# Optimization experiments

Measured on AMD Instinct MI355X. Metric: run time of the kernel, lower is better.

Reference implementation:

```python
import jax, jax.numpy as jnp
import numpy as np

N, E, B = 40000, 640000, 8192
IN, META, HID, OUT = 768, 6, 256, 128
NE, K, REL, NET = 4, 2, 200, 3
NL, NH, FF = 4, 4, 512


def setup_inputs():
    key = jax.random.key(0)
    keys = iter(jax.random.split(key, 64))
    def p(*shape):
        return jax.random.normal(next(keys), shape, jnp.float32) * 0.02
    return dict(
        x=jax.random.normal(next(keys), (N, IN + META), jnp.float32),
        noise=jax.random.normal(next(keys), (3, B, NE), jnp.float32),
        g_lin1_w=p(HID, IN + META), g_lin1_b=p(HID),
        conv_W=p(2, HID, HID), conv_Wr=p(2, HID, REL), conv_a=p(2, 3 * HID),
        conv_Wres=p(2, HID, HID), conv_rel=p(2, NET, REL),
        g_lin2_w=p(OUT, HID), g_lin2_b=p(OUT),
        te_w=p(OUT, IN), te_b=p(OUT),
        me_w1=p(HID, META), me_b1=p(HID), me_w2=p(OUT, HID), me_b2=p(OUT),
        moe_gate_w=p(3, NE, OUT), moe_noise_w=p(3, OUT),
        moe_w1=p(3, NE, 4 * OUT, OUT), moe_b1=p(3, NE, 4 * OUT),
        moe_w2=p(3, NE, OUT, 4 * OUT), moe_b2=p(3, NE, OUT),
        tf_qkv_w=p(NL, 3 * OUT, OUT), tf_qkv_b=p(NL, 3 * OUT),
        tf_out_w=p(NL, OUT, OUT), tf_out_b=p(NL, OUT),
        tf_ln1_g=jnp.ones((NL, OUT), jnp.float32), tf_ln1_b=jnp.zeros((NL, OUT), jnp.float32),
        tf_ff1_w=p(NL, FF, OUT), tf_ff1_b=p(NL, FF),
        tf_ff2_w=p(NL, OUT, FF), tf_ff2_b=p(NL, OUT),
        tf_ln2_g=jnp.ones((NL, OUT), jnp.float32), tf_ln2_b=jnp.zeros((NL, OUT), jnp.float32),
        clf_w=p(2, 3 * OUT), clf_b=p(2),
        edge_index=jax.random.randint(next(keys), (2, E), 0, N),
        edge_type=jax.random.randint(next(keys), (E,), 0, NET),
        batch_size=B,
    )


def _seg_softmax(logit, seg, n):
    m = jax.ops.segment_max(logit, seg, num_segments=n)
    e = jnp.exp(logit - m[seg])
    s = jax.ops.segment_sum(e, seg, num_segments=n)
    return e / (s[seg] + 1e-16)


def _hgn_layer(h, src, dst, et, W, Wr, a, Wres, rel, final):
    n, d = h.shape[0], W.shape[0]
    Wx = h @ W.T  # [N, HID]
    # a(cat(Wx_i, Wx_j, Wr_rel)) decomposed: per-node + per-edge-type scalars
    s_i = Wx @ a[:d]
    s_j = Wx @ a[d:2 * d]
    r_s = (rel @ Wr.T) @ a[2 * d:]  # [NET]
    logit = jax.nn.leaky_relu(s_i[dst] + s_j[src] + r_s[et], 0.2)
    alpha = _seg_softmax(logit, dst, n)
    agg = jax.ops.segment_sum(Wx[src] * alpha[:, None], dst, num_segments=n)
    out = jax.nn.elu(agg + h @ Wres.T)
    if final:
        out = out / jnp.maximum(jnp.linalg.norm(out, axis=1, keepdims=True), 1e-12)
    return out


def _moe(xv, eps, gate_w, noise_w, w1, b1, w2, b2):
    g = xv @ gate_w.T                       # [B, NE]
    nsd = jax.nn.softplus(xv @ noise_w)     # [B]
    h = g + eps * nsd[:, None]
    _, bot = jax.lax.top_k(-h, K)           # bottom-K experts get -inf
    drop = jnp.sum(jax.nn.one_hot(bot, NE, dtype=h.dtype), axis=1) > 0
    h = jnp.where(drop, -jnp.inf, h)
    L = jax.nn.softmax(h, axis=1)
    logits, idx = jax.lax.top_k(L, K)
    tmp = L.sum(0)
    loss = (jnp.std(tmp, ddof=1) / jnp.mean(tmp)) ** 2
    comb = jnp.einsum('bs,bse->be', logits, jax.nn.one_hot(idx, NE, dtype=L.dtype))
    h1 = jax.nn.relu(jnp.einsum('bd,ehd->ebh', xv, w1) + b1[:, None, :])
    eo = jnp.einsum('ebh,eoh->ebo', h1, w2) + b2[:, None, :]  # [NE, B, OUT]
    return jnp.einsum('be,ebo->bo', comb, eo), loss


def _ln(x, g, b):
    mu = x.mean(-1, keepdims=True)
    var = x.var(-1, keepdims=True)
    return (x - mu) / jnp.sqrt(var + 1e-5) * g + b


def _tf_layer(x, qkv_w, qkv_b, out_w, out_b, ln1g, ln1b, f1w, f1b, f2w, f2b, ln2g, ln2b):
    Bq, S, D = x.shape
    hd = D // NH
    qkv = x @ qkv_w.T + qkv_b
    q, k, v = jnp.split(qkv, 3, axis=-1)
    q = q.reshape(Bq, S, NH, hd)
    k = k.reshape(Bq, S, NH, hd)
    v = v.reshape(Bq, S, NH, hd)
    att = jax.nn.softmax(jnp.einsum('bshd,bthd->bhst', q, k) / jnp.sqrt(jnp.float32(hd)), axis=-1)
    o = jnp.einsum('bhst,bthd->bshd', att, v).reshape(Bq, S, D)
    x = _ln(x + o @ out_w.T + out_b, ln1g, ln1b)
    ff = jax.nn.relu(x @ f1w.T + f1b) @ f2w.T + f2b
    return _ln(x + ff, ln2g, ln2b)


def _forward(x, noise, g_lin1_w, g_lin1_b, conv_W, conv_Wr, conv_a, conv_Wres, conv_rel,
             g_lin2_w, g_lin2_b, te_w, te_b, me_w1, me_b1, me_w2, me_b2,
             moe_gate_w, moe_noise_w, moe_w1, moe_b1, moe_w2, moe_b2,
             tf_qkv_w, tf_qkv_b, tf_out_w, tf_out_b, tf_ln1_g, tf_ln1_b,
             tf_ff1_w, tf_ff1_b, tf_ff2_w, tf_ff2_b, tf_ln2_g, tf_ln2_b,
             clf_w, clf_b, edge_index, edge_type, batch_size):
    src, dst = edge_index[0], edge_index[1]
    # graph encoder (dropout is eval no-op)
    h = jax.nn.relu(x @ g_lin1_w.T + g_lin1_b)
    h = _hgn_layer(h, src, dst, edge_type, conv_W[0], conv_Wr[0], conv_a[0], conv_Wres[0], conv_rel[0], False)
    h = _hgn_layer(h, src, dst, edge_type, conv_W[1], conv_Wr[1], conv_a[1], conv_Wres[1], conv_rel[1], True)
    graph = jax.nn.relu(h @ g_lin2_w.T + g_lin2_b)
    x_g = graph[:batch_size]
    text = x[:batch_size, :IN]
    meta = x[:batch_size, IN:]
    x_t = jax.nn.relu(text @ te_w.T + te_b)
    x_m = jax.nn.relu(jax.nn.relu(meta @ me_w1.T + me_b1) @ me_w2.T + me_b2)
    outs, losses = [], []
    for i, xv in enumerate((x_g, x_t, x_m)):
        o, l = _moe(xv, noise[i], moe_gate_w[i], moe_noise_w[i], moe_w1[i], moe_b1[i], moe_w2[i], moe_b2[i])
        outs.append(o)
        losses.append(l)
    loss = losses[0] + losses[1] + losses[2]
    z = jnp.stack(outs, axis=1)  # [B, 3, OUT]
    for li in range(NL):
        z = _tf_layer(z, tf_qkv_w[li], tf_qkv_b[li], tf_out_w[li], tf_out_b[li],
                      tf_ln1_g[li], tf_ln1_b[li], tf_ff1_w[li], tf_ff1_b[li],
                      tf_ff2_w[li], tf_ff2_b[li], tf_ln2_g[li], tf_ln2_b[li])
    logits = z.reshape(z.shape[0], -1) @ clf_w.T + clf_b
    return logits, loss


def reference(x, noise, g_lin1_w, g_lin1_b, conv_W, conv_Wr, conv_a, conv_Wres, conv_rel,
              g_lin2_w, g_lin2_b, te_w, te_b, me_w1, me_b1, me_w2, me_b2,
              moe_gate_w, moe_noise_w, moe_w1, moe_b1, moe_w2, moe_b2,
              tf_qkv_w, tf_qkv_b, tf_out_w, tf_out_b, tf_ln1_g, tf_ln1_b,
              tf_ff1_w, tf_ff1_b, tf_ff2_w, tf_ff2_b, tf_ln2_g, tf_ln2_b,
              clf_w, clf_b, edge_index, edge_type, batch_size):
    return _forward(x, noise, g_lin1_w, g_lin1_b, conv_W, conv_Wr, conv_a, conv_Wres, conv_rel,
                    g_lin2_w, g_lin2_b, te_w, te_b, me_w1, me_b1, me_w2, me_b2,
                    moe_gate_w, moe_noise_w, moe_w1, moe_b1, moe_w2, moe_b2,
                    tf_qkv_w, tf_qkv_b, tf_out_w, tf_out_b, tf_ln1_g, tf_ln1_b,
                    tf_ff1_w, tf_ff1_b, tf_ff2_w, tf_ff2_b, tf_ln2_g, tf_ln2_b,
                    clf_w, clf_b, edge_index, edge_type, batch_size)
```

## Files before the change

### kernel.cpp

```cpp
#include <hip/hip_runtime.h>
#include <hip/hip_bf16.h>
#include <math.h>

#define NN 40000
#define EE 640000
#define BB 8192
#define IN_DIM 768
#define META_DIM 6
#define XDIM 774
#define HID 256
#define OUT_D 128
#define NEXP 4
#define NET_T 3
#define REL_D 200
#define NLAY 4
#define FF_D 512

typedef __attribute__((ext_vector_type(8))) short short8;
typedef __attribute__((ext_vector_type(4))) float f32x4;

__device__ __forceinline__ ushort f2bf(float f) {
    union { float f; unsigned u; } a; a.f = f;
    unsigned u = a.u;
    unsigned r = (u + 0x7FFFu + ((u >> 16) & 1u)) >> 16;
    return (ushort)r;
}
__device__ __forceinline__ float bf2f(ushort h) {
    union { unsigned u; float f; } a; a.u = ((unsigned)h) << 16;
    return a.f;
}

__global__ void cvt_kernel(const float* __restrict__ src, int ldsrc, int Kreal,
                           ushort* __restrict__ hi, ushort* __restrict__ lo,
                           int R, int ldp)
{
    size_t i = (size_t)blockIdx.x * blockDim.x + threadIdx.x;
    size_t total = (size_t)R * ldp;
    if (i >= total) return;
    int col = (int)(i % ldp);
    int row = (int)(i / ldp);
    float v = (col < Kreal) ? src[(size_t)row * ldsrc + col] : 0.f;
    ushort h = f2bf(v);
    float rem = v - bf2f(h);
    hi[i] = h;
    lo[i] = f2bf(rem);
}

static void cvt(const float* src, int ldsrc, int Kreal, ushort* hi, ushort* lo,
                int R, int ldp, hipStream_t s)
{
    size_t total = (size_t)R * ldp;
    cvt_kernel<<<(int)((total + 255) / 256), 256, 0, s>>>(src, ldsrc, Kreal, hi, lo, R, ldp);
}

template<int ACT, int HAS_RES>
__global__ __launch_bounds__(256) void mfma_gemm3(
    const ushort* __restrict__ Ahi, const ushort* __restrict__ Alo, int lda,
    const ushort* __restrict__ Bhi, const ushort* __restrict__ Blo, int ldb,
    const float* __restrict__ bias, const float* __restrict__ res,
    float* __restrict__ C, int M, int Nn, int K)
{
    __shared__ __align__(16) ushort Ash[128 * 40];
    __shared__ __align__(16) ushort Asl[128 * 40];
    __shared__ __align__(16) ushort Bsh[64 * 40];
    __shared__ __align__(16) ushort Bsl[64 * 40];

    int bn = blockIdx.x * 64;
    int bm = blockIdx.y * 128;
    int t = threadIdx.x;
    int wave = t >> 6, lane = t & 63;
    int wm = wave & 1, wn = wave >> 1;
    int quad = lane >> 4, r = lane & 15;

    f32x4 acc[4][2];
#pragma unroll
    for (int i = 0; i < 4; i++)
#pragma unroll
        for (int j = 0; j < 2; j++) acc[i][j] = (f32x4){0.f, 0.f, 0.f, 0.f};

    for (int k0 = 0; k0 < K; k0 += 32) {
#pragma unroll
        for (int i = 0; i < 2; i++) {
            int idx = t + i * 256;
            int row = idx >> 2, c8 = idx & 3;
            int grow = bm + row; if (grow > M - 1) grow = M - 1;
            size_t off = (size_t)grow * lda + k0 + c8 * 8;
            *(short8*)&Ash[row * 40 + c8 * 8] = *(const short8*)(Ahi + off);
            *(short8*)&Asl[row * 40 + c8 * 8] = *(const short8*)(Alo + off);
        }
        {
            int row = t >> 2, c8 = t & 3;
            size_t off = (size_t)(bn + row) * ldb + k0 + c8 * 8;
            *(short8*)&Bsh[row * 40 + c8 * 8] = *(const short8*)(Bhi + off);
            *(short8*)&Bsl[row * 40 + c8 * 8] = *(const short8*)(Blo + off);
        }
        __syncthreads();

        short8 ah[4], al[4], bh[2], bl[2];
#pragma unroll
        for (int i = 0; i < 4; i++) {
            int ro = (wm * 64 + i * 16 + r) * 40 + quad * 8;
            ah[i] = *(const short8*)&Ash[ro];
            al[i] = *(const short8*)&Asl[ro];
        }
#pragma unroll
        for (int j = 0; j < 2; j++) {
            int ro = (wn * 32 + j * 16 + r) * 40 + quad * 8;
            bh[j] = *(const short8*)&Bsh[ro];
            bl[j] = *(const short8*)&Bsl[ro];
        }
#pragma unroll
        for (int i = 0; i < 4; i++)
#pragma unroll
            for (int j = 0; j < 2; j++)
                acc[i][j] = __builtin_amdgcn_mfma_f32_16x16x32_bf16(ah[i], bh[j], acc[i][j], 0, 0, 0);
#pragma unroll
        for (int i = 0; i < 4; i++)
#pragma unroll
            for (int j = 0; j < 2; j++)
                acc[i][j] = __builtin_amdgcn_mfma_f32_16x16x32_bf16(ah[i], bl[j], acc[i][j], 0, 0, 0);
#pragma unroll
        for (int i = 0; i < 4; i++)
#pragma unroll
            for (int j = 0; j < 2; j++)
                acc[i][j] = __builtin_amdgcn_mfma_f32_16x16x32_bf16(al[i], bh[j], acc[i][j], 0, 0, 0);
        __syncthreads();
    }

    float bcol[2];
#pragma unroll
    for (int j = 0; j < 2; j++)
        bcol[j] = bias ? bias[bn + wn * 32 + j * 16 + r] : 0.f;
#pragma unroll
    for (int i = 0; i < 4; i++) {
#pragma unroll
        for (int j = 0; j < 2; j++) {
            int col = bn + wn * 32 + j * 16 + r;
#pragma unroll
            for (int reg = 0; reg < 4; reg++) {
                int row = bm + wm * 64 + i * 16 + quad * 4 + reg;
                if (row >= M) continue;
                float v = acc[i][j][reg] + bcol[j];
                if (HAS_RES) v += res[(size_t)row * Nn + col];
                if (ACT == 1) v = fmaxf(v, 0.f);
                else if (ACT == 2) v = (v > 0.f) ? v : expm1f(v);
                C[(size_t)row * Nn + col] = v;
            }
        }
    }
}

template<int ACT, int HAS_RES>
static void mfma3_launch(const ushort* Ahi, const ushort* Alo, int lda,
                         const ushort* Bhi, const ushort* Blo, int ldb,
                         const float* bias, const float* res, float* C,
                         int M, int Nn, int K, hipStream_t s)
{
    dim3 grid(Nn / 64, (M + 127) / 128);
    mfma_gemm3<ACT, HAS_RES><<<grid, 256, 0, s>>>(Ahi, Alo, lda, Bhi, Blo, ldb,
                                                  bias, res, C, M, Nn, K);
}

template<int ACT>
__global__ void gemm_kernel(const float* __restrict__ A, int lda,
                            const float* __restrict__ Bw,
                            const float* __restrict__ bias,
                            const float* __restrict__ res,
                            float* __restrict__ C, int M, int Nn, int K)
{
    __shared__ float As[16][68];
    __shared__ float Bs[16][68];
    int bm = blockIdx.y * 64, bn = blockIdx.x * 64;
    int t = threadIdx.x;
    int tx = t & 15, ty = t >> 4;
    float acc[4][4] = {{0.f}};

    for (int k0 = 0; k0 < K; k0 += 16) {
#pragma unroll
        for (int i = 0; i < 4; i++) {
            int l = t * 4 + i; int mm = l >> 4, kk = l & 15;
            int gm = bm + mm, gk = k0 + kk;
            As[kk][mm] = (gm < M && gk < K) ? A[(size_t)gm * lda + gk] : 0.f;
        }
#pragma unroll
        for (int i = 0; i < 4; i++) {
            int l = t * 4 + i; int nn = l >> 4, kk = l & 15;
            int gn = bn + nn, gk = k0 + kk;
            Bs[kk][nn] = (gn < Nn && gk < K) ? Bw[(size_t)gn * K + gk] : 0.f;
        }
        __syncthreads();
#pragma unroll
        for (int kk = 0; kk < 16; kk++) {
            float4 a4 = *reinterpret_cast<const float4*>(&As[kk][ty * 4]);
            float4 b4 = *reinterpret_cast<const float4*>(&Bs[kk][tx * 4]);
            float a0[4] = {a4.x, a4.y, a4.z, a4.w};
            float b0[4] = {b4.x, b4.y, b4.z, b4.w};
#pragma unroll
            for (int i = 0; i < 4; i++)
#pragma unroll
                for (int j = 0; j < 4; j++)
                    acc[i][j] += a0[i] * b0[j];
        }
        __syncthreads();
    }
#pragma unroll
    for (int i = 0; i < 4; i++) {
        int gm = bm + ty * 4 + i; if (gm >= M) continue;
#pragma unroll
        for (int j = 0; j < 4; j++) {
            int gn = bn + tx * 4 + j; if (gn >= Nn) continue;
            float v = acc[i][j];
            if (bias) v += bias[gn];
            if (res)  v += res[(size_t)gm * Nn + gn];
            if (ACT == 1) v = fmaxf(v, 0.f);
            else if (ACT == 2) v = (v > 0.f) ? v : expm1f(v);
            C[(size_t)gm * Nn + gn] = v;
        }
    }
}

static void launch_gemm(int act, const float* A, int lda, const float* Bw,
                        const float* bias, const float* res, float* C,
                        int M, int Nn, int K, hipStream_t s)
{
    dim3 grid((Nn + 63) / 64, (M + 63) / 64);
    dim3 blk(256);
    if (act == 0)      gemm_kernel<0><<<grid, blk, 0, s>>>(A, lda, Bw, bias, res, C, M, Nn, K);
    else if (act == 1) gemm_kernel<1><<<grid, blk, 0, s>>>(A, lda, Bw, bias, res, C, M, Nn, K);
    else               gemm_kernel<2><<<grid, blk, 0, s>>>(A, lda, Bw, bias, res, C, M, Nn, K);
}

template<int ACT, int A_BF16, int OUT_BF16>
__global__ __launch_bounds__(256) void mfma_gemm(
    const void* __restrict__ Ap, size_t strideAz,
    const float* __restrict__ Bw, size_t strideBz,
    const float* __restrict__ bias, size_t strideBiasz,
    void* __restrict__ Cp, size_t strideCz,
    int M, int Nn, int K)
{
    __shared__ __align__(16) ushort As[128 * 40];
    __shared__ __align__(16) ushort Bs[64 * 40];

    int z = blockIdx.z;
// ... 142 lines not shown
        buf[t] = v;
        __syncthreads();
        for (int off = 1; off < 1024; off <<= 1) {
            int x = (t >= off) ? buf[t - off] : 0;
            __syncthreads();
            buf[t] += x;
            __syncthreads();
        }
        int incl = buf[t];
        int base = carry;
        if (c + t < n) { rowstart[c + t] = base + incl - v; cursor[c + t] = base + incl - v; }
        __syncthreads();
        if (t == 1023) carry = base + incl;
        __syncthreads();
    }
    if (t == 0) rowstart[n] = carry;
}

__global__ void fill_kernel(const int* __restrict__ src, const int* __restrict__ dst,
                            const int* __restrict__ et, int* __restrict__ cursor,
                            unsigned* __restrict__ csr_val)
{
    int e = blockIdx.x * blockDim.x + threadIdx.x;
    if (e >= EE) return;
    int d = dst[e];
    int pos = atomicAdd(&cursor[d], 1);
    csr_val[pos] = (unsigned)src[e] | ((unsigned)et[e] << 16);
}

__global__ void csr_agg_kernel(const unsigned* __restrict__ csr_val,
                               const int* __restrict__ rowstart,
                               const float* __restrict__ s_i, const float* __restrict__ s_j,
                               const float* __restrict__ rsv,
                               const float* __restrict__ Wx, float* __restrict__ agg)
{
    int t = threadIdx.x; int w = t >> 6, l = t & 63;
    int node = blockIdx.x * 4 + w; if (node >= NN) return;
    int start = rowstart[node], end = rowstart[node + 1];
    float r0 = rsv[0], r1 = rsv[1], r2 = rsv[2];
    float si = s_i[node];

    float m = -INFINITY;
    for (int i = start + l; i < end; i += 64) {
        unsigned v = csr_val[i];
        int s = v & 0xFFFF; int et = v >> 16;
        float rr = (et == 0) ? r0 : ((et == 1) ? r1 : r2);
        float lg = si + s_j[s] + rr;
        lg = (lg >= 0.f) ? lg : 0.2f * lg;
        m = fmaxf(m, lg);
    }
    for (int off = 32; off; off >>= 1) m = fmaxf(m, __shfl_down(m, off));
    m = __shfl(m, 0);

    float a0 = 0.f, a1 = 0.f, a2 = 0.f, a3 = 0.f, ssum = 0.f;
    for (int c = start; c < end; c += 64) {
        int nchunk = min(64, end - c);
        float wgt = 0.f; int sidx = 0;
        if (l < nchunk) {
            unsigned v = csr_val[c + l];
            sidx = v & 0xFFFF; int et = v >> 16;
            float rr = (et == 0) ? r0 : ((et == 1) ? r1 : r2);
            float lg = si + s_j[sidx] + rr;
            lg = (lg >= 0.f) ? lg : 0.2f * lg;
            wgt = expf(lg - m);
            ssum += wgt;
        }
        for (int j = 0; j < nchunk; j++) {
            float wj = __shfl(wgt, j);
            int sj = __shfl(sidx, j);
            const float* wr = Wx + (size_t)sj * HID;
            a0 += wj * wr[l];
            a1 += wj * wr[l + 64];
            a2 += wj * wr[l + 128];
            a3 += wj * wr[l + 192];
        }
    }
    for (int off = 32; off; off >>= 1) ssum += __shfl_down(ssum, off);
    ssum = __shfl(ssum, 0);
    float inv = 1.f / (ssum + 1e-16f);
    float* ar = agg + (size_t)node * HID;
    ar[l] = a0 * inv; ar[l + 64] = a1 * inv; ar[l + 128] = a2 * inv; ar[l + 192] = a3 * inv;
}

__global__ void rownorm_kernel(float* __restrict__ h, int n)
{
    int t = threadIdx.x; int w = t >> 6, l = t & 63;
    int m = blockIdx.x * 4 + w; if (m >= n) return;
    float* r = h + (size_t)m * HID;
    float vals[4]; float q = 0.f;
#pragma unroll
    for (int i = 0; i < 4; i++) { vals[i] = r[l + 64 * i]; q += vals[i] * vals[i]; }
    for (int off = 32; off; off >>= 1) q += __shfl_down(q, off);
    q = __shfl(q, 0);
    float inv = 1.f / fmaxf(sqrtf(q), 1e-12f);
#pragma unroll
    for (int i = 0; i < 4; i++) r[l + 64 * i] = vals[i] * inv;
}

__global__ void moe_gate_kernel(const float* __restrict__ xv, const float* __restrict__ gate_w,
                                const float* __restrict__ noise_w, const float* __restrict__ eps,
                                float* __restrict__ comb, float* __restrict__ tmpsum)
{
    __shared__ float part[4];
    int t = threadIdx.x; int w = t >> 6, l = t & 63;
    if (t < 4) part[t] = 0.f;
    __syncthreads();
    int b = blockIdx.x * 4 + w;
    const float* xr = xv + (size_t)b * OUT_D;
    float x0 = xr[l], x1 = xr[l + 64];
    float dots[5];
#pragma unroll
    for (int e = 0; e < 4; e++) {
        const float* gw = gate_w + e * OUT_D;
        float v = x0 * gw[l] + x1 * gw[l + 64];
        for (int off = 32; off; off >>= 1) v += __shfl_down(v, off);
        dots[e] = v;
    }
    {
        float v = x0 * noise_w[l] + x1 * noise_w[l + 64];
        for (int off = 32; off; off >>= 1) v += __shfl_down(v, off);
        dots[4] = v;
    }
    if (l == 0) {
        float xg = dots[4];
        float nsd = (xg > 20.f) ? xg : log1pf(expf(xg));
        float hv[4];
#pragma unroll
        for (int e = 0; e < 4; e++) hv[e] = dots[e] + eps[(size_t)b * 4 + e] * nsd;
        int i1 = 0;
        for (int e = 1; e < 4; e++) if (hv[e] < hv[i1]) i1 = e;
        int i2 = -1;
        for (int e = 0; e < 4; e++) { if (e == i1) continue; if (i2 < 0 || hv[e] < hv[i2]) i2 = e; }
        int k1 = -1, k2 = -1;
        for (int e = 0; e < 4; e++) { if (e != i1 && e != i2) { if (k1 < 0) k1 = e; else k2 = e; } }
        float mm = fmaxf(hv[k1], hv[k2]);
        float e1 = expf(hv[k1] - mm), e2 = expf(hv[k2] - mm);
        float s = e1 + e2;
        float L[4] = {0.f, 0.f, 0.f, 0.f};
        L[k1] = e1 / s; L[k2] = e2 / s;
#pragma unroll
        for (int e = 0; e < 4; e++) comb[(size_t)b * 4 + e] = L[e];
        atomicAdd(&part[k1], L[k1]);
        atomicAdd(&part[k2], L[k2]);
    }
    __syncthreads();
    if (t < 4) atomicAdd(&tmpsum[t], part[t]);
}

__global__ void moe_combine_kernel(const float* __restrict__ eo, const float* __restrict__ comb,
                                   float* __restrict__ zout)
{
    int idx = blockIdx.x * blockDim.x + threadIdx.x;
    if (idx >= BB * OUT_D) return;
    int b = idx >> 7, o = idx & 127;
    const size_t S = (size_t)BB * OUT_D;
    float v = comb[b * 4 + 0] * eo[idx] + comb[b * 4 + 1] * eo[idx + S]
            + comb[b * 4 + 2] * eo[idx + 2 * S] + comb[b * 4 + 3] * eo[idx + 3 * S];
    zout[(size_t)b * (3 * OUT_D) + o] = v;
}

__global__ void loss_kernel(const float* __restrict__ tmpsum, float* __restrict__ out)
{
    if (threadIdx.x == 0 && blockIdx.x == 0) {
        float total = 0.f;
        for (int v = 0; v < 3; v++) {
            const float* tp = tmpsum + v * 4;
            float mean = (tp[0] + tp[1] + tp[2] + tp[3]) * 0.25f;
            float var = 0.f;
            for (int e = 0; e < 4; e++) { float d = tp[e] - mean; var += d * d; }
            var /= 3.f;
            float r = sqrtf(var) / mean;
            total += r * r;
        }
        out[0] = total;
    }
}

__global__ void attn_kernel(const float* __restrict__ qkv, float* __restrict__ o)
{
// ... 42 lines not shown
    float v0 = xr[l] + ar[l], v1 = xr[l + 64] + ar[l + 64];
    float s = v0 + v1;
    for (int off = 32; off; off >>= 1) s += __shfl_down(s, off);
    s = __shfl(s, 0);
    float mu = s * (1.f / 128.f);
    float d0 = v0 - mu, d1 = v1 - mu;
    float q = d0 * d0 + d1 * d1;
    for (int off = 32; off; off >>= 1) q += __shfl_down(q, off);
    q = __shfl(q, 0);
    float inv = rsqrtf(q * (1.f / 128.f) + 1e-5f);
    xr[l]      = d0 * inv * g[l] + bta[l];
    xr[l + 64] = d1 * inv * g[l + 64] + bta[l + 64];
}

__global__ void clf_kernel(const float* __restrict__ z, const float* __restrict__ w,
                           const float* __restrict__ b, float* __restrict__ out)
{
    int t = threadIdx.x; int wv = t >> 6, l = t & 63;
    int row = blockIdx.x * 4 + wv; if (row >= BB) return;
    const float* zr = z + (size_t)row * 384;
    float v0 = 0.f, v1 = 0.f;
    for (int i = l; i < 384; i += 64) {
        float zz = zr[i];
        v0 += zz * w[i];
        v1 += zz * w[384 + i];
    }
    for (int off = 32; off; off >>= 1) { v0 += __shfl_down(v0, off); v1 += __shfl_down(v1, off); }
    if (l == 0) { out[row * 2] = v0 + b[0]; out[row * 2 + 1] = v1 + b[1]; }
}

extern "C" void kernel_launch(void* const* d_in, const int* in_sizes, int n_in,
                              void* d_out, int out_size, void* d_ws, size_t ws_size,
                              hipStream_t stream)
{
    const float* x         = (const float*)d_in[0];
    const float* noise     = (const float*)d_in[1];
    const float* g_lin1_w  = (const float*)d_in[2];
    const float* g_lin1_b  = (const float*)d_in[3];
    const float* conv_W    = (const float*)d_in[4];
    const float* conv_Wr   = (const float*)d_in[5];
    const float* conv_a    = (const float*)d_in[6];
    const float* conv_Wres = (const float*)d_in[7];
    const float* conv_rel  = (const float*)d_in[8];
    const float* g_lin2_w  = (const float*)d_in[9];
    const float* g_lin2_b  = (const float*)d_in[10];
    const float* te_w      = (const float*)d_in[11];
    const float* te_b      = (const float*)d_in[12];
    const float* me_w1     = (const float*)d_in[13];
    const float* me_b1     = (const float*)d_in[14];
    const float* me_w2     = (const float*)d_in[15];
    const float* me_b2     = (const float*)d_in[16];
    const float* moe_gate_w  = (const float*)d_in[17];
    const float* moe_noise_w = (const float*)d_in[18];
    const float* moe_w1    = (const float*)d_in[19];
    const float* moe_b1    = (const float*)d_in[20];
    const float* moe_w2    = (const float*)d_in[21];
    const float* moe_b2    = (const float*)d_in[22];
    const float* tf_qkv_w  = (const float*)d_in[23];
    const float* tf_qkv_b  = (const float*)d_in[24];
    const float* tf_out_w  = (const float*)d_in[25];
    const float* tf_out_b  = (const float*)d_in[26];
    const float* tf_ln1_g  = (const float*)d_in[27];
    const float* tf_ln1_b  = (const float*)d_in[28];
    const float* tf_ff1_w  = (const float*)d_in[29];
    const float* tf_ff1_b  = (const float*)d_in[30];
    const float* tf_ff2_w  = (const float*)d_in[31];
    const float* tf_ff2_b  = (const float*)d_in[32];
    const float* tf_ln2_g  = (const float*)d_in[33];
    const float* tf_ln2_b  = (const float*)d_in[34];
    const float* clf_w     = (const float*)d_in[35];
    const float* clf_b     = (const float*)d_in[36];
    const int*   edge_index = (const int*)d_in[37];
    const int*   edge_type  = (const int*)d_in[38];

    float* ws = (float*)d_ws;

    const size_t F_A = 0;
    const size_t F_B = 10240000;
    const size_t F_C = 22822912;
    const size_t F_D = 33062912;
    const size_t F_M = 43302912;
    const size_t F_X = 44200000;

    float* h0     = ws + F_A;
    float* qkv    = ws + F_A;
    float* wx     = ws + F_B;
    float* graph  = ws + F_B;
    ushort* ff1bf = (ushort*)(ws + F_B);
    float* agg    = ws + F_C;
    float* x_mh   = ws + F_C;
    ushort* h1bf  = (ushort*)(ws + F_C);
    float* attn_o = ws + F_C;
    float* tmp1   = ws + F_C + 3200000;
    float* hl1    = ws + F_D;
    float* z      = ws + F_D;
    float* x_t    = ws + F_D + 3200000;
    float* x_m    = ws + F_D + 4300000;
    float* eo     = ws + F_D + 5400000;

    float* s_i    = ws + F_M;
    float* s_j    = ws + F_M + 40000;
    float* rsv    = ws + F_M + 80000;
    float* comb   = ws + F_M + 80016;
    float* tmpsum = ws + F_M + 112784;
    int* deg      = (int*)(ws + F_M + 120000);
    int* rowstart = (int*)(ws + F_M + 161000);
    int* cursor   = (int*)(ws + F_M + 202000);
    unsigned* csr_val = (unsigned*)(ws + F_M + 242000);

    ushort* xhi = (ushort*)(ws + F_X);
    ushort* xlo = (ushort*)(ws + F_X + 16000000);
    ushort* hhi = (ushort*)(ws + F_X + 32000000);
    ushort* hlo = (ushort*)(ws + F_X + 37120000);
    ushort* wbh = (ushort*)(ws + F_X + 42240000);
    ushort* wbl = (ushort*)(ws + F_X + 42342400);

    const int* srcv = edge_index;
    const int* dstv = edge_index + EE;

    hipMemsetAsync(deg, 0, NN * sizeof(int), stream);
    deg_kernel<<<(EE + 255) / 256, 256, 0, stream>>>(dstv, deg);
    scan_kernel<<<1, 1024, 0, stream>>>(deg, rowstart, cursor, NN);
    fill_kernel<<<(EE + 255) / 256, 256, 0, stream>>>(srcv, dstv, edge_type, cursor, csr_val);

    cvt(x, XDIM, XDIM, xhi, xlo, NN, 800, stream);
    cvt(g_lin1_w, XDIM, XDIM, wbh, wbl, HID, 800, stream);
    mfma3_launch<1, 0>(xhi, xlo, 800, wbh, wbl, 800, g_lin1_b, nullptr, h0,
                       NN, HID, 800, stream);

    float* hin = h0;
    float* hout = hl1;
    for (int layer = 0; layer < 2; layer++) {
        const float* W    = conv_W    + (size_t)layer * HID * HID;
        const float* Wr   = conv_Wr   + (size_t)layer * HID * REL_D;
        const float* a    = conv_a    + (size_t)layer * 3 * HID;
        const float* Wres = conv_Wres + (size_t)layer * HID * HID;
        const float* rel  = conv_rel  + (size_t)layer * NET_T * REL_D;

        cvt(hin, HID, HID, hhi, hlo, NN, HID, stream);
        cvt(W, HID, HID, wbh, wbl, HID, HID, stream);
        mfma3_launch<0, 0>(hhi, hlo, HID, wbh, wbl, HID, nullptr, nullptr, wx,
                           NN, HID, HID, stream);
        sisj_kernel<<<NN / 4, 256, 0, stream>>>(wx, a, s_i, s_j, NN);
        rs_kernel<<<NET_T, 256, 0, stream>>>(Wr, rel, a + 2 * HID, rsv);
        csr_agg_kernel<<<NN / 4, 256, 0, stream>>>(csr_val, rowstart, s_i, s_j, rsv, wx, agg);
        cvt(Wres, HID, HID, wbh, wbl, HID, HID, stream);
        mfma3_launch<2, 1>(hhi, hlo, HID, wbh, wbl, HID, nullptr, agg, hout,
                           NN, HID, HID, stream);
        if (layer == 1) rownorm_kernel<<<NN / 4, 256, 0, stream>>>(hout, NN);
        float* t2 = hin; hin = hout; hout = t2;
    }
    float* h2 = hin;

    cvt(h2, HID, HID, hhi, hlo, NN, HID, stream);
    cvt(g_lin2_w, HID, HID, wbh, wbl, OUT_D, HID, stream);
    mfma3_launch<1, 0>(hhi, hlo, HID, wbh, wbl, HID, g_lin2_b, nullptr, graph,
                       NN, OUT_D, HID, stream);

    cvt(te_w, IN_DIM, IN_DIM, wbh, wbl, OUT_D, IN_DIM, stream);
    mfma3_launch<1, 0>(xhi, xlo, 800, wbh, wbl, IN_DIM, te_b, nullptr, x_t,
                       BB, OUT_D, IN_DIM, stream);
    launch_gemm(1, x + IN_DIM, XDIM, me_w1, me_b1, nullptr, x_mh, BB, HID, META_DIM, stream);
    launch_gemm(1, x_mh, HID, me_w2, me_b2, nullptr, x_m, BB, OUT_D, HID, stream);

    hipMemsetAsync(tmpsum, 0, 16 * sizeof(float), stream);
    const float* xvs[3] = { graph, x_t, x_m };
    for (int v = 0; v < 3; v++) {
        const float* xv = xvs[v];
        moe_gate_kernel<<<BB / 4, 256, 0, stream>>>(
            xv, moe_gate_w + (size_t)v * NEXP * OUT_D, moe_noise_w + (size_t)v * OUT_D,
            noise + (size_t)v * BB * NEXP, comb, tmpsum + v * 4);
        mfma_launch<1, 0, 1>(xv, 0,
                             moe_w1 + (size_t)v * 4 * FF_D * OUT_D, (size_t)FF_D * OUT_D,
                             moe_b1 + (size_t)v * 4 * FF_D, FF_D,
                             h1bf, (size_t)BB * FF_D,
                             BB, FF_D, OUT_D, 4, stream);
        mfma_launch<0, 1, 0>(h1bf, (size_t)BB * FF_D,
                             moe_w2 + (size_t)v * 4 * OUT_D * FF_D, (size_t)OUT_D * FF_D,
                             moe_b2 + (size_t)v * 4 * OUT_D, OUT_D,
                             eo, (size_t)BB * OUT_D,
                             BB, OUT_D, FF_D, 4, stream);
        moe_combine_kernel<<<(BB * OUT_D) / 256, 256, 0, stream>>>(eo, comb, z + v * OUT_D);
    }

    const int MT = BB * 3;
    for (int li = 0; li < NLAY; li++) {
        mfma_launch<0, 0, 0>(z, 0, tf_qkv_w + (size_t)li * 384 * 128, 0,
                             tf_qkv_b + li * 384, 0, qkv, 0, MT, 384, 128, 1, stream);
        attn_kernel<<<(BB * 4) / 8, 256, 0, stream>>>(qkv, attn_o);
        mfma_launch<0, 0, 0>(attn_o, 0, tf_out_w + (size_t)li * 128 * 128, 0,
                             tf_out_b + li * 128, 0, tmp1, 0, MT, 128, 128, 1, stream);
        ln_residual_kernel<<<MT / 4, 256, 0, stream>>>(z, tmp1, tf_ln1_g + li * 128, tf_ln1_b + li * 128, MT);
        mfma_launch<1, 0, 1>(z, 0, tf_ff1_w + (size_t)li * 512 * 128, 0,
                             tf_ff1_b + li * 512, 0, ff1bf, 0, MT, 512, 128, 1, stream);
        mfma_launch<0, 1, 0>(ff1bf, 0, tf_ff2_w + (size_t)li * 128 * 512, 0,
                             tf_ff2_b + li * 128, 0, tmp1, 0, MT, 128, 512, 1, stream);
        ln_residual_kernel<<<MT / 4, 256, 0, stream>>>(z, tmp1, tf_ln2_g + li * 128, tf_ln2_b + li * 128, MT);
    }

    clf_kernel<<<BB / 4, 256, 0, stream>>>(z, clf_w, clf_b, (float*)d_out);
    loss_kernel<<<1, 64, 0, stream>>>(tmpsum, (float*)d_out + BB * 2);
}
```

Before: 1.875 ms.

## Fuse bf16 hi/lo split into GEMM epilogues and add full-width N=256 tile

Adds a GEMM kernel whose 64x256 tile covers all 256 output columns, so each A row tile is loaded once. Its epilogue can write the hi/lo bf16 split directly. Node features are now kept in split form between graph layers, which removes the separate cvt passes over the 40000x256 activations. The row normalisation now works on the split buffers. The meta-encoder second linear moves from the scalar GEMM to the 3xbf16 MFMA path. This costs a larger shared-memory footprint per block and reorganises workspace offsets.

```diff
diff --git a/kernel.cpp b/kernel.cpp
--- a/kernel.cpp
+++ b/kernel.cpp
@@ -53,6 +53,110 @@
     cvt_kernel<<<(int)((total + 255) / 256), 256, 0, s>>>(src, ldsrc, Kreal, hi, lo, R, ldp);
 }
 
+template<int ACT, int HAS_RES, int OUT_SPLIT>
+__global__ __launch_bounds__(256) void mfma3_n256(
+    const ushort* __restrict__ Ahi, const ushort* __restrict__ Alo, int lda,
+    const ushort* __restrict__ Bhi, const ushort* __restrict__ Blo, int ldb,
+    const float* __restrict__ bias, const float* __restrict__ res,
+    float* __restrict__ C, ushort* __restrict__ Chi, ushort* __restrict__ Clo,
+    int M, int K)
+{
+    __shared__ __align__(16) ushort Ash[64 * 40];
+    __shared__ __align__(16) ushort Asl[64 * 40];
+    __shared__ __align__(16) ushort Bsh[256 * 40];
+    __shared__ __align__(16) ushort Bsl[256 * 40];
+
+    int bm = blockIdx.x * 64;
+    int t = threadIdx.x;
+    int wv = t >> 6, lane = t & 63;
+    int quad = lane >> 4, r = lane & 15;
+
+    f32x4 acc[4][4];
+#pragma unroll
+    for (int i = 0; i < 4; i++)
+#pragma unroll
+        for (int j = 0; j < 4; j++) acc[i][j] = (f32x4){0.f, 0.f, 0.f, 0.f};
+
+    for (int k0 = 0; k0 < K; k0 += 32) {
+        {
+            int row = t >> 2, c8 = t & 3;
+            int grow = bm + row; if (grow > M - 1) grow = M - 1;
+            size_t off = (size_t)grow * lda + k0 + c8 * 8;
+            *(short8*)&Ash[row * 40 + c8 * 8] = *(const short8*)(Ahi + off);
+            *(short8*)&Asl[row * 40 + c8 * 8] = *(const short8*)(Alo + off);
+        }
+#pragma unroll
+        for (int i = 0; i < 4; i++) {
+            int idx = t + i * 256;
+            int row = idx >> 2, c8 = idx & 3;
+            size_t off = (size_t)row * ldb + k0 + c8 * 8;
+            *(short8*)&Bsh[row * 40 + c8 * 8] = *(const short8*)(Bhi + off);
+            *(short8*)&Bsl[row * 40 + c8 * 8] = *(const short8*)(Blo + off);
+        }
+        __syncthreads();
+
+        short8 ah[4], al[4];
+#pragma unroll
+        for (int i = 0; i < 4; i++) {
+            int ro = (i * 16 + r) * 40 + quad * 8;
+            ah[i] = *(const short8*)&Ash[ro];
+            al[i] = *(const short8*)&Asl[ro];
+        }
+#pragma unroll
+        for (int j = 0; j < 4; j++) {
+            int ro = (wv * 64 + j * 16 + r) * 40 + quad * 8;
+            short8 bh = *(const short8*)&Bsh[ro];
+            short8 bl = *(const short8*)&Bsl[ro];
+#pragma unroll
+            for (int i = 0; i < 4; i++)
+                acc[i][j] = __builtin_amdgcn_mfma_f32_16x16x32_bf16(ah[i], bh, acc[i][j], 0, 0, 0);
+#pragma unroll
+            for (int i = 0; i < 4; i++)
+                acc[i][j] = __builtin_amdgcn_mfma_f32_16x16x32_bf16(ah[i], bl, acc[i][j], 0, 0, 0);
+#pragma unroll
+            for (int i = 0; i < 4; i++)
+                acc[i][j] = __builtin_amdgcn_mfma_f32_16x16x32_bf16(al[i], bh, acc[i][j], 0, 0, 0);
+        }
+        __syncthreads();
+    }
+
+#pragma unroll
+    for (int j = 0; j < 4; j++) {
+        int col = wv * 64 + j * 16 + r;
+        float bc = bias ? bias[col] : 0.f;
+#pragma unroll
+        for (int i = 0; i < 4; i++) {
+#pragma unroll
+            for (int reg = 0; reg < 4; reg++) {
+                int row = bm + i * 16 + quad * 4 + reg;
+                if (row >= M) continue;
+                float v = acc[i][j][reg] + bc;
+                if (HAS_RES) v += res[(size_t)row * 256 + col];
+                if (ACT == 1) v = fmaxf(v, 0.f);
+                else if (ACT == 2) v = (v > 0.f) ? v : expm1f(v);
+                if (OUT_SPLIT) {
+                    ushort h = f2bf(v);
+                    Chi[(size_t)row * 256 + col] = h;
+                    Clo[(size_t)row * 256 + col] = f2bf(v - bf2f(h));
+                } else {
+                    C[(size_t)row * 256 + col] = v;
+                }
+            }
+        }
+    }
+}
+
+template<int ACT, int HAS_RES, int OUT_SPLIT>
+static void n256_launch(const ushort* Ahi, const ushort* Alo, int lda,
+                        const ushort* Bhi, const ushort* Blo, int ldb,
+                        const float* bias, const float* res,
+                        float* C, ushort* Chi, ushort* Clo,
+                        int M, int K, hipStream_t s)
+{
+    mfma3_n256<ACT, HAS_RES, OUT_SPLIT><<<(M + 63) / 64, 256, 0, s>>>(
+        Ahi, Alo, lda, Bhi, Blo, ldb, bias, res, C, Chi, Clo, M, K);
+}
+
 template<int ACT, int HAS_RES>
 __global__ __launch_bounds__(256) void mfma_gemm3(
     const ushort* __restrict__ Ahi, const ushort* __restrict__ Alo, int lda,
@@ -467,19 +571,27 @@
     ar[l] = a0 * inv; ar[l + 64] = a1 * inv; ar[l + 128] = a2 * inv; ar[l + 192] = a3 * inv;
 }
 
-__global__ void rownorm_kernel(float* __restrict__ h, int n)
+__global__ void rownorm_split(ushort* __restrict__ hi, ushort* __restrict__ lo, int n)
 {
     int t = threadIdx.x; int w = t >> 6, l = t & 63;
     int m = blockIdx.x * 4 + w; if (m >= n) return;
-    float* r = h + (size_t)m * HID;
+    size_t base = (size_t)m * HID;
     float vals[4]; float q = 0.f;
 #pragma unroll
-    for (int i = 0; i < 4; i++) { vals[i] = r[l + 64 * i]; q += vals[i] * vals[i]; }
+    for (int i = 0; i < 4; i++) {
+        vals[i] = bf2f(hi[base + l + 64 * i]) + bf2f(lo[base + l + 64 * i]);
+        q += vals[i] * vals[i];
+    }
     for (int off = 32; off; off >>= 1) q += __shfl_down(q, off);
     q = __shfl(q, 0);
     float inv = 1.f / fmaxf(sqrtf(q), 1e-12f);
 #pragma unroll
-    for (int i = 0; i < 4; i++) r[l + 64 * i] = vals[i] * inv;
+    for (int i = 0; i < 4; i++) {
+        float nv = vals[i] * inv;
+        ushort h = f2bf(nv);
+        hi[base + l + 64 * i] = h;
+        lo[base + l + 64 * i] = f2bf(nv - bf2f(h));
+    }
 }
 
 __global__ void moe_gate_kernel(const float* __restrict__ xv, const float* __restrict__ gate_w,
@@ -688,7 +800,8 @@
     const size_t F_M = 43302912;
     const size_t F_X = 44200000;
 
-    float* h0     = ws + F_A;
+    ushort* hAhi  = (ushort*)(ws + F_A);
+    ushort* hAlo  = (ushort*)(ws + F_A + 5120000);
     float* qkv    = ws + F_A;
     float* wx     = ws + F_B;
     float* graph  = ws + F_B;
@@ -698,7 +811,8 @@
     ushort* h1bf  = (ushort*)(ws + F_C);
     float* attn_o = ws + F_C;
     float* tmp1   = ws + F_C + 3200000;
-    float* hl1    = ws + F_D;
+    ushort* hBhi  = (ushort*)(ws + F_D);
+    ushort* hBlo  = (ushort*)(ws + F_D + 5120000);
     float* z      = ws + F_D;
     float* x_t    = ws + F_D + 3200000;
     float* x_m    = ws + F_D + 4300000;
@@ -714,12 +828,12 @@
     int* cursor   = (int*)(ws + F_M + 202000);
     unsigned* csr_val = (unsigned*)(ws + F_M + 242000);
 
-    ushort* xhi = (ushort*)(ws + F_X);
-    ushort* xlo = (ushort*)(ws + F_X + 16000000);
-    ushort* hhi = (ushort*)(ws + F_X + 32000000);
-    ushort* hlo = (ushort*)(ws + F_X + 37120000);
-    ushort* wbh = (ushort*)(ws + F_X + 42240000);
-    ushort* wbl = (ushort*)(ws + F_X + 42342400);
+    ushort* xhi  = (ushort*)(ws + F_X);
+    ushort* xlo  = (ushort*)(ws + F_X + 16000000);
+    ushort* wbh  = (ushort*)(ws + F_X + 32000000);
+    ushort* wbl  = (ushort*)(ws + F_X + 32110000);
+    ushort* mhhi = (ushort*)(ws + F_X + 32220000);
+    ushort* mhlo = (ushort*)(ws + F_X + 33280000);
 
     const int* srcv = edge_index;
     const int* dstv = edge_index + EE;
@@ -731,11 +845,10 @@
 
     cvt(x, XDIM, XDIM, xhi, xlo, NN, 800, stream);
     cvt(g_lin1_w, XDIM, XDIM, wbh, wbl, HID, 800, stream);
-    mfma3_launch<1, 0>(xhi, xlo, 800, wbh, wbl, 800, g_lin1_b, nullptr, h0,
-                       NN, HID, 800, stream);
-
-    float* hin = h0;
-    float* hout = hl1;
+    n256_launch<1, 0, 1>(xhi, xlo, 800, wbh, wbl, 800, g_lin1_b, nullptr,
+                         nullptr, hAhi, hAlo, NN, 800, stream);
+
+    ushort *inhi = hAhi, *inlo = hAlo, *outhi = hBhi, *outlo = hBlo;
     for (int layer = 0; layer < 2; layer++) {
         const float* W    = conv_W    + (size_t)layer * HID * HID;
         const float* Wr   = conv_Wr   + (size_t)layer * HID * REL_D;
@@ -743,31 +856,32 @@
         const float* Wres = conv_Wres + (size_t)layer * HID * HID;
         const float* rel  = conv_rel  + (size_t)layer * NET_T * REL_D;
 
-        cvt(hin, HID, HID, hhi, hlo, NN, HID, stream);
         cvt(W, HID, HID, wbh, wbl, HID, HID, stream);
-        mfma3_launch<0, 0>(hhi, hlo, HID, wbh, wbl, HID, nullptr, nullptr, wx,
-                           NN, HID, HID, stream);
+        n256_launch<0, 0, 0>(inhi, inlo, HID, wbh, wbl, HID, nullptr, nullptr,
+                             wx, nullptr, nullptr, NN, HID, stream);
         sisj_kernel<<<NN / 4, 256, 0, stream>>>(wx, a, s_i, s_j, NN);
         rs_kernel<<<NET_T, 256, 0, stream>>>(Wr, rel, a + 2 * HID, rsv);
         csr_agg_kernel<<<NN / 4, 256, 0, stream>>>(csr_val, rowstart, s_i, s_j, rsv, wx, agg);
         cvt(Wres, HID, HID, wbh, wbl, HID, HID, stream);
-        mfma3_launch<2, 1>(hhi, hlo, HID, wbh, wbl, HID, nullptr, agg, hout,
-                           NN, HID, HID, stream);
-        if (layer == 1) rownorm_kernel<<<NN / 4, 256, 0, stream>>>(hout, NN);
-        float* t2 = hin; hin = hout; hout = t2;
-    }
-    float* h2 = hin;
-
-    cvt(h2, HID, HID, hhi, hlo, NN, HID, stream);
+        n256_launch<2, 1, 1>(inhi, inlo, HID, wbh, wbl, HID, nullptr, agg,
+                             nullptr, outhi, outlo, NN, HID, stream);
+        ushort* th = inhi; inhi = outhi; outhi = th;
+        ushort* tl = inlo; inlo = outlo; outlo = tl;
+    }
+    rownorm_split<<<NN / 4, 256, 0, stream>>>(inhi, inlo, NN);
+
     cvt(g_lin2_w, HID, HID, wbh, wbl, OUT_D, HID, stream);
-    mfma3_launch<1, 0>(hhi, hlo, HID, wbh, wbl, HID, g_lin2_b, nullptr, graph,
+    mfma3_launch<1, 0>(inhi, inlo, HID, wbh, wbl, HID, g_lin2_b, nullptr, graph,
                        NN, OUT_D, HID, stream);
 
     cvt(te_w, IN_DIM, IN_DIM, wbh, wbl, OUT_D, IN_DIM, stream);
     mfma3_launch<1, 0>(xhi, xlo, 800, wbh, wbl, IN_DIM, te_b, nullptr, x_t,
                        BB, OUT_D, IN_DIM, stream);
     launch_gemm(1, x + IN_DIM, XDIM, me_w1, me_b1, nullptr, x_mh, BB, HID, META_DIM, stream);
-    launch_gemm(1, x_mh, HID, me_w2, me_b2, nullptr, x_m, BB, OUT_D, HID, stream);
+    cvt(x_mh, HID, HID, mhhi, mhlo, BB, HID, stream);
+    cvt(me_w2, HID, HID, wbh, wbl, OUT_D, HID, stream);
+    mfma3_launch<1, 0>(mhhi, mhlo, HID, wbh, wbl, HID, me_b2, nullptr, x_m,
+                       BB, OUT_D, HID, stream);
 
     hipMemsetAsync(tmpsum, 0, 16 * sizeof(float), stream);
     const float* xvs[3] = { graph, x_t, x_m };
```

After: 1.937 ms. +3.3%, slower.

## Widen split-bf16 MFMA GEMM tile and emit hi/lo outputs directly

Applied to the files above, without the earlier changes.

The split-bf16 MFMA GEMM tile grows from 128x64 to 128x128, so each wave computes a 64x64 subtile and the A tile is reused across more columns. Epilogues of the GNN GEMMs can now write the hi/lo bf16 pair directly, which removes the separate fp32-to-split conversion passes on node features between layers. Row normalization now runs on the split representation. The meta-encoder second linear also moves from the fp32 SIMT GEMM to the MFMA path, at the cost of an extra conversion pass and more registers and LDS per block, which may lower occupancy.

```diff
diff --git a/kernel.cpp b/kernel.cpp
--- a/kernel.cpp
+++ b/kernel.cpp
@@ -53,30 +53,31 @@
     cvt_kernel<<<(int)((total + 255) / 256), 256, 0, s>>>(src, ldsrc, Kreal, hi, lo, R, ldp);
 }
 
-template<int ACT, int HAS_RES>
-__global__ __launch_bounds__(256) void mfma_gemm3(
+template<int ACT, int HAS_RES, int OUT_SPLIT>
+__global__ __launch_bounds__(256) void mfma3_128(
     const ushort* __restrict__ Ahi, const ushort* __restrict__ Alo, int lda,
     const ushort* __restrict__ Bhi, const ushort* __restrict__ Blo, int ldb,
     const float* __restrict__ bias, const float* __restrict__ res,
-    float* __restrict__ C, int M, int Nn, int K)
+    float* __restrict__ C, ushort* __restrict__ Chi, ushort* __restrict__ Clo,
+    int M, int Nn, int K)
 {
     __shared__ __align__(16) ushort Ash[128 * 40];
     __shared__ __align__(16) ushort Asl[128 * 40];
-    __shared__ __align__(16) ushort Bsh[64 * 40];
-    __shared__ __align__(16) ushort Bsl[64 * 40];
-
-    int bn = blockIdx.x * 64;
+    __shared__ __align__(16) ushort Bsh[128 * 40];
+    __shared__ __align__(16) ushort Bsl[128 * 40];
+
+    int bn = blockIdx.x * 128;
     int bm = blockIdx.y * 128;
     int t = threadIdx.x;
     int wave = t >> 6, lane = t & 63;
     int wm = wave & 1, wn = wave >> 1;
     int quad = lane >> 4, r = lane & 15;
 
-    f32x4 acc[4][2];
+    f32x4 acc[4][4];
 #pragma unroll
     for (int i = 0; i < 4; i++)
 #pragma unroll
-        for (int j = 0; j < 2; j++) acc[i][j] = (f32x4){0.f, 0.f, 0.f, 0.f};
+        for (int j = 0; j < 4; j++) acc[i][j] = (f32x4){0.f, 0.f, 0.f, 0.f};
 
     for (int k0 = 0; k0 < K; k0 += 32) {
 #pragma unroll
@@ -88,15 +89,17 @@
             *(short8*)&Ash[row * 40 + c8 * 8] = *(const short8*)(Ahi + off);
             *(short8*)&Asl[row * 40 + c8 * 8] = *(const short8*)(Alo + off);
         }
-        {
-            int row = t >> 2, c8 = t & 3;
+#pragma unroll
+        for (int i = 0; i < 2; i++) {
+            int idx = t + i * 256;
+            int row = idx >> 2, c8 = idx & 3;
             size_t off = (size_t)(bn + row) * ldb + k0 + c8 * 8;
             *(short8*)&Bsh[row * 40 + c8 * 8] = *(const short8*)(Bhi + off);
             *(short8*)&Bsl[row * 40 + c8 * 8] = *(const short8*)(Blo + off);
         }
         __syncthreads();
 
-        short8 ah[4], al[4], bh[2], bl[2];
+        short8 ah[4], al[4], bh[4], bl[4];
 #pragma unroll
         for (int i = 0; i < 4; i++) {
             int ro = (wm * 64 + i * 16 + r) * 40 + quad * 8;
@@ -104,61 +107,65 @@
             al[i] = *(const short8*)&Asl[ro];
         }
 #pragma unroll
-        for (int j = 0; j < 2; j++) {
-            int ro = (wn * 32 + j * 16 + r) * 40 + quad * 8;
+        for (int j = 0; j < 4; j++) {
+            int ro = (wn * 64 + j * 16 + r) * 40 + quad * 8;
             bh[j] = *(const short8*)&Bsh[ro];
             bl[j] = *(const short8*)&Bsl[ro];
         }
 #pragma unroll
-        for (int i = 0; i < 4; i++)
-#pragma unroll
-            for (int j = 0; j < 2; j++)
+        for (int j = 0; j < 4; j++)
+#pragma unroll
+            for (int i = 0; i < 4; i++)
                 acc[i][j] = __builtin_amdgcn_mfma_f32_16x16x32_bf16(ah[i], bh[j], acc[i][j], 0, 0, 0);
 #pragma unroll
-        for (int i = 0; i < 4; i++)
-#pragma unroll
-            for (int j = 0; j < 2; j++)
+        for (int j = 0; j < 4; j++)
+#pragma unroll
+            for (int i = 0; i < 4; i++)
                 acc[i][j] = __builtin_amdgcn_mfma_f32_16x16x32_bf16(ah[i], bl[j], acc[i][j], 0, 0, 0);
 #pragma unroll
-        for (int i = 0; i < 4; i++)
-#pragma unroll
-            for (int j = 0; j < 2; j++)
+        for (int j = 0; j < 4; j++)
+#pragma unroll
+            for (int i = 0; i < 4; i++)
                 acc[i][j] = __builtin_amdgcn_mfma_f32_16x16x32_bf16(al[i], bh[j], acc[i][j], 0, 0, 0);
         __syncthreads();
     }
 
-    float bcol[2];
-#pragma unroll
-    for (int j = 0; j < 2; j++)
-        bcol[j] = bias ? bias[bn + wn * 32 + j * 16 + r] : 0.f;
-#pragma unroll
-    for (int i = 0; i < 4; i++) {
-#pragma unroll
-        for (int j = 0; j < 2; j++) {
-            int col = bn + wn * 32 + j * 16 + r;
+#pragma unroll
+    for (int j = 0; j < 4; j++) {
+        int col = bn + wn * 64 + j * 16 + r;
+        float bc = bias ? bias[col] : 0.f;
+#pragma unroll
+        for (int i = 0; i < 4; i++) {
 #pragma unroll
             for (int reg = 0; reg < 4; reg++) {
                 int row = bm + wm * 64 + i * 16 + quad * 4 + reg;
                 if (row >= M) continue;
-                float v = acc[i][j][reg] + bcol[j];
+                float v = acc[i][j][reg] + bc;
                 if (HAS_RES) v += res[(size_t)row * Nn + col];
                 if (ACT == 1) v = fmaxf(v, 0.f);
                 else if (ACT == 2) v = (v > 0.f) ? v : expm1f(v);
-                C[(size_t)row * Nn + col] = v;
+                if (OUT_SPLIT) {
+                    ushort h = f2bf(v);
+                    Chi[(size_t)row * Nn + col] = h;
+                    Clo[(size_t)row * Nn + col] = f2bf(v - bf2f(h));
+                } else {
+                    C[(size_t)row * Nn + col] = v;
+                }
             }
         }
     }
 }
 
-template<int ACT, int HAS_RES>
-static void mfma3_launch(const ushort* Ahi, const ushort* Alo, int lda,
-                         const ushort* Bhi, const ushort* Blo, int ldb,
-                         const float* bias, const float* res, float* C,
-                         int M, int Nn, int K, hipStream_t s)
-{
-    dim3 grid(Nn / 64, (M + 127) / 128);
-    mfma_gemm3<ACT, HAS_RES><<<grid, 256, 0, s>>>(Ahi, Alo, lda, Bhi, Blo, ldb,
-                                                  bias, res, C, M, Nn, K);
+template<int ACT, int HAS_RES, int OUT_SPLIT>
+static void m128_launch(const ushort* Ahi, const ushort* Alo, int lda,
+                        const ushort* Bhi, const ushort* Blo, int ldb,
+                        const float* bias, const float* res,
+                        float* C, ushort* Chi, ushort* Clo,
+                        int M, int Nn, int K, hipStream_t s)
+{
+    dim3 grid(Nn / 128, (M + 127) / 128);
+    mfma3_128<ACT, HAS_RES, OUT_SPLIT><<<grid, 256, 0, s>>>(
+        Ahi, Alo, lda, Bhi, Blo, ldb, bias, res, C, Chi, Clo, M, Nn, K);
 }
 
 template<int ACT>
@@ -467,19 +474,27 @@
     ar[l] = a0 * inv; ar[l + 64] = a1 * inv; ar[l + 128] = a2 * inv; ar[l + 192] = a3 * inv;
 }
 
-__global__ void rownorm_kernel(float* __restrict__ h, int n)
+__global__ void rownorm_split(ushort* __restrict__ hi, ushort* __restrict__ lo, int n)
 {
     int t = threadIdx.x; int w = t >> 6, l = t & 63;
     int m = blockIdx.x * 4 + w; if (m >= n) return;
-    float* r = h + (size_t)m * HID;
+    size_t base = (size_t)m * HID;
     float vals[4]; float q = 0.f;
 #pragma unroll
-    for (int i = 0; i < 4; i++) { vals[i] = r[l + 64 * i]; q += vals[i] * vals[i]; }
+    for (int i = 0; i < 4; i++) {
+        vals[i] = bf2f(hi[base + l + 64 * i]) + bf2f(lo[base + l + 64 * i]);
+        q += vals[i] * vals[i];
+    }
     for (int off = 32; off; off >>= 1) q += __shfl_down(q, off);
     q = __shfl(q, 0);
     float inv = 1.f / fmaxf(sqrtf(q), 1e-12f);
 #pragma unroll
-    for (int i = 0; i < 4; i++) r[l + 64 * i] = vals[i] * inv;
+    for (int i = 0; i < 4; i++) {
+        float nv = vals[i] * inv;
+        ushort h = f2bf(nv);
+        hi[base + l + 64 * i] = h;
+        lo[base + l + 64 * i] = f2bf(nv - bf2f(h));
+    }
 }
 
 __global__ void moe_gate_kernel(const float* __restrict__ xv, const float* __restrict__ gate_w,
@@ -688,7 +703,8 @@
     const size_t F_M = 43302912;
     const size_t F_X = 44200000;
 
-    float* h0     = ws + F_A;
+    ushort* hAhi  = (ushort*)(ws + F_A);
+    ushort* hAlo  = (ushort*)(ws + F_A + 5120000);
     float* qkv    = ws + F_A;
     float* wx     = ws + F_B;
     float* graph  = ws + F_B;
@@ -698,7 +714,8 @@
     ushort* h1bf  = (ushort*)(ws + F_C);
     float* attn_o = ws + F_C;
     float* tmp1   = ws + F_C + 3200000;
-    float* hl1    = ws + F_D;
+    ushort* hBhi  = (ushort*)(ws + F_D);
+    ushort* hBlo  = (ushort*)(ws + F_D + 5120000);
     float* z      = ws + F_D;
     float* x_t    = ws + F_D + 3200000;
     float* x_m    = ws + F_D + 4300000;
@@ -714,12 +731,12 @@
     int* cursor   = (int*)(ws + F_M + 202000);
     unsigned* csr_val = (unsigned*)(ws + F_M + 242000);
 
-    ushort* xhi = (ushort*)(ws + F_X);
-    ushort* xlo = (ushort*)(ws + F_X + 16000000);
-    ushort* hhi = (ushort*)(ws + F_X + 32000000);
-    ushort* hlo = (ushort*)(ws + F_X + 37120000);
-    ushort* wbh = (ushort*)(ws + F_X + 42240000);
-    ushort* wbl = (ushort*)(ws + F_X + 42342400);
+    ushort* xhi  = (ushort*)(ws + F_X);
+    ushort* xlo  = (ushort*)(ws + F_X + 16000000);
+    ushort* wbh  = (ushort*)(ws + F_X + 32000000);
+    ushort* wbl  = (ushort*)(ws + F_X + 32110000);
+    ushort* mhhi = (ushort*)(ws + F_X + 32220000);
+    ushort* mhlo = (ushort*)(ws + F_X + 33280000);
 
     const int* srcv = edge_index;
     const int* dstv = edge_index + EE;
@@ -731,11 +748,10 @@
 
     cvt(x, XDIM, XDIM, xhi, xlo, NN, 800, stream);
     cvt(g_lin1_w, XDIM, XDIM, wbh, wbl, HID, 800, stream);
-    mfma3_launch<1, 0>(xhi, xlo, 800, wbh, wbl, 800, g_lin1_b, nullptr, h0,
-                       NN, HID, 800, stream);
-
-    float* hin = h0;
-    float* hout = hl1;
+    m128_launch<1, 0, 1>(xhi, xlo, 800, wbh, wbl, 800, g_lin1_b, nullptr,
+                         nullptr, hAhi, hAlo, NN, HID, 800, stream);
+
+    ushort *inhi = hAhi, *inlo = hAlo, *outhi = hBhi, *outlo = hBlo;
     for (int layer = 0; layer < 2; layer++) {
         const float* W    = conv_W    + (size_t)layer * HID * HID;
         const float* Wr   = conv_Wr   + (size_t)layer * HID * REL_D;
@@ -743,31 +759,32 @@
         const float* Wres = conv_Wres + (size_t)layer * HID * HID;
         const float* rel  = conv_rel  + (size_t)layer * NET_T * REL_D;
 
-        cvt(hin, HID, HID, hhi, hlo, NN, HID, stream);
         cvt(W, HID, HID, wbh, wbl, HID, HID, stream);
-        mfma3_launch<0, 0>(hhi, hlo, HID, wbh, wbl, HID, nullptr, nullptr, wx,
-                           NN, HID, HID, stream);
+        m128_launch<0, 0, 0>(inhi, inlo, HID, wbh, wbl, HID, nullptr, nullptr,
+                             wx, nullptr, nullptr, NN, HID, HID, stream);
         sisj_kernel<<<NN / 4, 256, 0, stream>>>(wx, a, s_i, s_j, NN);
         rs_kernel<<<NET_T, 256, 0, stream>>>(Wr, rel, a + 2 * HID, rsv);
         csr_agg_kernel<<<NN / 4, 256, 0, stream>>>(csr_val, rowstart, s_i, s_j, rsv, wx, agg);
         cvt(Wres, HID, HID, wbh, wbl, HID, HID, stream);
-        mfma3_launch<2, 1>(hhi, hlo, HID, wbh, wbl, HID, nullptr, agg, hout,
-                           NN, HID, HID, stream);
-        if (layer == 1) rownorm_kernel<<<NN / 4, 256, 0, stream>>>(hout, NN);
-        float* t2 = hin; hin = hout; hout = t2;
-    }
-    float* h2 = hin;
-
-    cvt(h2, HID, HID, hhi, hlo, NN, HID, stream);
+        m128_launch<2, 1, 1>(inhi, inlo, HID, wbh, wbl, HID, nullptr, agg,
+                             nullptr, outhi, outlo, NN, HID, HID, stream);
+        ushort* th = inhi; inhi = outhi; outhi = th;
+        ushort* tl = inlo; inlo = outlo; outlo = tl;
+    }
+    rownorm_split<<<NN / 4, 256, 0, stream>>>(inhi, inlo, NN);
+
     cvt(g_lin2_w, HID, HID, wbh, wbl, OUT_D, HID, stream);
-    mfma3_launch<1, 0>(hhi, hlo, HID, wbh, wbl, HID, g_lin2_b, nullptr, graph,
-                       NN, OUT_D, HID, stream);
+    m128_launch<1, 0, 0>(inhi, inlo, HID, wbh, wbl, HID, g_lin2_b, nullptr,
+                         graph, nullptr, nullptr, NN, OUT_D, HID, stream);
 
     cvt(te_w, IN_DIM, IN_DIM, wbh, wbl, OUT_D, IN_DIM, stream);
-    mfma3_launch<1, 0>(xhi, xlo, 800, wbh, wbl, IN_DIM, te_b, nullptr, x_t,
-                       BB, OUT_D, IN_DIM, stream);
+    m128_launch<1, 0, 0>(xhi, xlo, 800, wbh, wbl, IN_DIM, te_b, nullptr,
+                         x_t, nullptr, nullptr, BB, OUT_D, IN_DIM, stream);
     launch_gemm(1, x + IN_DIM, XDIM, me_w1, me_b1, nullptr, x_mh, BB, HID, META_DIM, stream);
-    launch_gemm(1, x_mh, HID, me_w2, me_b2, nullptr, x_m, BB, OUT_D, HID, stream);
+    cvt(x_mh, HID, HID, mhhi, mhlo, BB, HID, stream);
+    cvt(me_w2, HID, HID, wbh, wbl, OUT_D, HID, stream);
+    m128_launch<1, 0, 0>(mhhi, mhlo, HID, wbh, wbl, HID, me_b2, nullptr,
+                         x_m, nullptr, nullptr, BB, OUT_D, HID, stream);
 
     hipMemsetAsync(tmpsum, 0, 16 * sizeof(float), stream);
     const float* xvs[3] = { graph, x_t, x_m };
```

After: 1.877 ms. Within noise of the previous version (+0.1%).
